# Optimization experiments

Hardware: AMD Instinct MI355X
Metric: run time of the kernel (lower is better)

The kernel has to match this reference:

```python
import jax, jax.numpy as jnp
import numpy as np

N = 50000
E = 1600000
F_IN = 512
H1, C1 = 8, 8          # layer1: 8 heads x 8 channels, concat -> 64
C2 = 40                # layer2: 1 head, num_classes
NEG_SLOPE = 0.2


def setup_inputs() -> dict:
    key = jax.random.key(0)
    ks = jax.random.split(key, 12)
    x = jax.random.normal(ks[0], (N, F_IN), dtype=jnp.float32)
    edge_index = jax.random.randint(ks[1], (2, E), 0, N, dtype=jnp.int32)
    s1 = 1.0 / np.sqrt(F_IN)
    W1 = jax.random.uniform(ks[2], (F_IN, H1 * C1), jnp.float32, -s1, s1)
    att_src1 = jax.random.normal(ks[3], (1, H1, C1), dtype=jnp.float32) * 0.1
    att_dst1 = jax.random.normal(ks[4], (1, H1, C1), dtype=jnp.float32) * 0.1
    b1 = jnp.zeros((H1 * C1,), jnp.float32)
    s2 = 1.0 / np.sqrt(H1 * C1)
    W2 = jax.random.uniform(ks[5], (H1 * C1, C2), jnp.float32, -s2, s2)
    att_src2 = jax.random.normal(ks[6], (1, 1, C2), dtype=jnp.float32) * 0.1
    att_dst2 = jax.random.normal(ks[7], (1, 1, C2), dtype=jnp.float32) * 0.1
    b2 = jnp.zeros((C2,), jnp.float32)
    return {"x": x, "edge_index": edge_index,
            "W1": W1, "att_src1": att_src1, "att_dst1": att_dst1, "b1": b1,
            "W2": W2, "att_src2": att_src2, "att_dst2": att_dst2, "b2": b2}


def gat_conv(x, W, att_src, att_dst, bias, src, dst, heads, out_ch, concat):
    n = x.shape[0]
    h = (x @ W).reshape(n, heads, out_ch)                 # [N,H,C]
    a_src = (h * att_src).sum(-1)                          # [N,H]
    a_dst = (h * att_dst).sum(-1)                          # [N,H]
    logits = jax.nn.leaky_relu(a_src[src] + a_dst[dst], NEG_SLOPE)  # [E,H]
    # segment softmax over incoming edges per destination node
    m = jax.ops.segment_max(logits, dst, num_segments=n)   # [N,H]
    ex = jnp.exp(logits - m[dst])                          # [E,H]
    denom = jax.ops.segment_sum(ex, dst, num_segments=n)   # [N,H]
    w = ex / denom[dst]                                    # [E,H]
    out = jax.ops.segment_sum(h[src] * w[:, :, None], dst, num_segments=n)  # [N,H,C]
    if concat:
        out = out.reshape(n, heads * out_ch)
    else:
        out = out.mean(axis=1)
    return out + bias


def reference(x, edge_index, W1, att_src1, att_dst1, b1, W2, att_src2, att_dst2, b2):
    # add self loops (PyG add_self_loops=True)
    loop = jnp.arange(N, dtype=edge_index.dtype)
    src = jnp.concatenate([edge_index[0], loop])
    dst = jnp.concatenate([edge_index[1], loop])
    # dropout is identity in eval mode
    h = gat_conv(x, W1, att_src1, att_dst1, b1, src, dst, H1, C1, True)
    h = jax.nn.relu(h)
    h = gat_conv(h, W2, att_src2, att_dst2, b2, src, dst, 1, C2, False)
    return jax.nn.log_softmax(h, axis=1)
```

## Files before the change

### kernel.cpp

```cpp
#include <hip/hip_runtime.h>
#include <math.h>

#define NN 50000
#define EE 1600000
#define FIN 512
#define H1N 8
#define C2N 40
#define NEG 0.2f

#define NB 391
#define CAPG 6144
#define PA_ITEMS 8192
#define NITEMS (EE + NN)
#define PA_BLOCKS ((NITEMS + PA_ITEMS - 1) / PA_ITEMS)

__global__ __launch_bounds__(256) void passA_kernel(const int* __restrict__ ei,
    int* __restrict__ bucket_cnt, unsigned int* __restrict__ bucket_glob) {
  __shared__ int hist[NB];
  __shared__ int prefix[NB];
  __shared__ int cursor[NB];
  __shared__ int gbase[NB];
  __shared__ int scA[512], scB[512];
  __shared__ unsigned int staging[PA_ITEMS];
  int t = threadIdx.x;
  int i0 = blockIdx.x * PA_ITEMS;
  int count = NITEMS - i0; if (count > PA_ITEMS) count = PA_ITEMS;

  for (int b = t; b < NB; b += 256) hist[b] = 0;
  __syncthreads();
  for (int j = t; j < count; j += 256) {
    int e = i0 + j;
    int dst = (e < EE) ? ei[EE + e] : (e - EE);
    atomicAdd(&hist[dst >> 7], 1);
  }
  __syncthreads();
  scA[t]       = (t < NB) ? hist[t] : 0;
  scA[t + 256] = (t + 256 < NB) ? hist[t + 256] : 0;
  __syncthreads();
  {
    int* pa = scA; int* pb = scB;
    for (int off = 1; off < 512; off <<= 1) {
      pb[t]       = pa[t]       + (t >= off ? pa[t - off] : 0);
      pb[t + 256] = pa[t + 256] + (t + 256 >= off ? pa[t + 256 - off] : 0);
      __syncthreads();
      int* tmp = pa; pa = pb; pb = tmp;
    }
    for (int b = t; b < NB; b += 256) {
      int ex = pa[b] - hist[b];
      prefix[b] = ex;
      cursor[b] = ex;
      if (hist[b] > 0) gbase[b] = atomicAdd(&bucket_cnt[b], hist[b]);
    }
  }
  __syncthreads();
  for (int j = t; j < count; j += 256) {
    int e = i0 + j;
    int src, dst;
    if (e < EE) { src = ei[e]; dst = ei[EE + e]; }
    else        { src = e - EE; dst = src; }
    int b = dst >> 7;
    unsigned int v = (unsigned int)src | ((unsigned int)(dst & 127) << 16)
                   | ((unsigned int)b << 23);
    int lp = atomicAdd(&cursor[b], 1);
    staging[lp] = v;
  }
  __syncthreads();
  for (int j = t; j < count; j += 256) {
    unsigned int v = staging[j];
    int b = (int)(v >> 23);
    int gpos = b * CAPG + gbase[b] + (j - prefix[b]);
    bucket_glob[gpos] = v;
  }
}

__global__ __launch_bounds__(512) void scan_buckets(const int* __restrict__ bucket_cnt,
    int* __restrict__ bucket_base, int* __restrict__ row_ptr_last) {
  __shared__ int scA[512], scB[512];
  int t = threadIdx.x;
  int v = (t < NB) ? bucket_cnt[t] : 0;
  scA[t] = v;
  __syncthreads();
  int* pa = scA; int* pb = scB;
  for (int off = 1; off < 512; off <<= 1) {
    pb[t] = pa[t] + (t >= off ? pa[t - off] : 0);
    __syncthreads();
    int* tmp = pa; pa = pb; pb = tmp;
  }
  if (t < NB) bucket_base[t] = pa[t] - v;
  if (t == NB - 1) *row_ptr_last = pa[t];
}

#define CAPB 6144
__global__ __launch_bounds__(256) void passB_kernel(const unsigned int* __restrict__ bucket_glob,
    const int* __restrict__ bucket_cnt, const int* __restrict__ bucket_base,
    int* __restrict__ row_ptr, int* __restrict__ col) {
  __shared__ int hist[128], pre[128], cur[128];
  __shared__ int scA[128], scB[128];
  __shared__ int sorted[CAPB];
  int b = blockIdx.x, t = threadIdx.x;
  int cnt = bucket_cnt[b];
  int base = bucket_base[b];
  const unsigned int* in = bucket_glob + (size_t)b * CAPG;
  if (t < 128) hist[t] = 0;
  __syncthreads();
  for (int j = t; j < cnt; j += 256) {
    int dl = (int)((in[j] >> 16) & 127u);
    atomicAdd(&hist[dl], 1);
  }
  __syncthreads();
  if (t < 128) scA[t] = hist[t];
  __syncthreads();
  {
    int* pa = scA; int* pb = scB;
    for (int off = 1; off < 128; off <<= 1) {
      if (t < 128) pb[t] = pa[t] + (t >= off ? pa[t - off] : 0);
      __syncthreads();
      int* tmp = pa; pa = pb; pb = tmp;
    }
    if (t < 128) {
      int ex = pa[t] - hist[t];
      pre[t] = ex;
      cur[t] = ex;
      int d = b * 128 + t;
      if (d < NN) row_ptr[d] = base + ex;
    }
  }
  __syncthreads();
  for (int j = t; j < cnt; j += 256) {
    unsigned int v = in[j];
    int dl = (int)((v >> 16) & 127u);
    int lp = atomicAdd(&cur[dl], 1);
    sorted[lp] = (int)(v & 0xFFFFu);
  }
  __syncthreads();
  for (int j = t; j < cnt; j += 256) col[base + j] = sorted[j];
}


typedef __attribute__((ext_vector_type(8))) short bf16x8;
typedef __attribute__((ext_vector_type(4))) float f32x4;

__device__ inline short f2bf(float f) {
  unsigned int u = __float_as_uint(f);
  u += 0x7FFFu + ((u >> 16) & 1u);
  return (short)(u >> 16);
}
__device__ inline unsigned int pack2bf(float lo, float hi) {
  return (unsigned int)(unsigned short)f2bf(lo) | ((unsigned int)(unsigned short)f2bf(hi) << 16);
}
__device__ inline float bflo(unsigned int v) { return __uint_as_float(v << 16); }
__device__ inline float bfhi(unsigned int v) { return __uint_as_float(v & 0xFFFF0000u); }


__global__ void w1t_kernel(const float* __restrict__ W, short* __restrict__ WT) {
  int i = blockIdx.x * 256 + threadIdx.x;
  if (i >= 64 * 512) return;
  int n = i >> 9, k = i & 511;
  WT[i] = f2bf(W[k * 64 + n]);
}

#define XS_STRIDE 136
__global__ __launch_bounds__(256) void gemm1_kernel(const float* __restrict__ x,
    const short* __restrict__ WT, unsigned short* __restrict__ h1b) {
  __shared__ short xs[64 * XS_STRIDE];
  int t = threadIdx.x;
  int wave = t >> 6, lane = t & 63;
  int quad = lane >> 4, m = lane & 15;
  int row0 = blockIdx.x * 64;
  f32x4 acc[4] = {{0.f,0.f,0.f,0.f},{0.f,0.f,0.f,0.f},{0.f,0.f,0.f,0.f},{0.f,0.f,0.f,0.f}};
  for (int kc = 0; kc < 4; ++kc) {
    int k0 = kc * 128;
    __syncthreads();
#pragma unroll
    for (int jj = 0; jj < 8; ++jj) {
      int idx = jj * 256 + t;
      int row = idx >> 5, kq = idx & 31;
      int rr = row0 + row; if (rr >= NN) rr = NN - 1;
      float4 v = *(const float4*)(x + (size_t)rr * FIN + k0 + kq * 4);
      short4 s;
      s.x = f2bf(v.x); s.y = f2bf(v.y); s.z = f2bf(v.z); s.w = f2bf(v.w);
      *(short4*)&xs[row * XS_STRIDE + kq * 4] = s;
    }
    __syncthreads();
#pragma unroll
    for (int ks = 0; ks < 4; ++ks) {
      bf16x8 a = *(bf16x8*)&xs[(wave * 16 + m) * XS_STRIDE + ks * 32 + quad * 8];
#pragma unroll
      for (int tl = 0; tl < 4; ++tl) {
        bf16x8 b = *(const bf16x8*)(WT + (size_t)(tl * 16 + m) * 512 + k0 + ks * 32 + quad * 8);
        acc[tl] = __builtin_amdgcn_mfma_f32_16x16x32_bf16(a, b, acc[tl], 0, 0, 0);
      }
    }
  }
  int rbase = row0 + wave * 16 + quad * 4;
#pragma unroll
  for (int tl = 0; tl < 4; ++tl) {
#pragma unroll
    for (int r = 0; r < 4; ++r) {
      int rr = rbase + r;
      if (rr < NN) h1b[(size_t)rr * 64 + tl * 16 + m] = (unsigned short)f2bf(acc[tl][r]);
    }
  }
}


__global__ void att1_kernel(const unsigned int* __restrict__ h1b, const float* __restrict__ att_src,
    const float* __restrict__ att_dst, float* __restrict__ asrc, float* __restrict__ adst) {
  int i = blockIdx.x * blockDim.x + threadIdx.x;
  if (i >= NN * H1N) return;
  int h = i & 7;
  uint4 v = *(const uint4*)(h1b + (size_t)i * 4);
  float f[8] = {bflo(v.x), bfhi(v.x), bflo(v.y), bfhi(v.y),
                bflo(v.z), bfhi(v.z), bflo(v.w), bfhi(v.w)};
  const float* as = att_src + h * 8;
  const float* ad = att_dst + h * 8;
  float s = 0.f, d = 0.f;
#pragma unroll
  for (int c = 0; c < 8; ++c) { s = fmaf(f[c], as[c], s); d = fmaf(f[c], ad[c], d); }
  asrc[i] = s;
  adst[i] = d;
}


__global__ __launch_bounds__(256) void l1_edge_kernel(const int* __restrict__ row_ptr,
    const int* __restrict__ col, const unsigned int* __restrict__ h1b,
    const float* __restrict__ asrc, const float* __restrict__ adst,
    const float* __restrict__ b1, float* __restrict__ hrelu) {
  int d = (blockIdx.x * blockDim.x + threadIdx.x) >> 6;
  int lane = threadIdx.x & 63;
  if (d >= NN) return;
  int half = lane >> 5, c2 = lane & 31, h = c2 >> 2;
  int start = row_ptr[d], end = row_ptr[d + 1];
  float adst_h = adst[d * 8 + h];
  float ax = 0.f, ay = 0.f, den = 0.f;
  int e = start;
  int n8 = start + ((end - start) & ~7);
  for (; e < n8; e += 8) {
    int s[4];
#pragma unroll
    for (int j = 0; j < 4; ++j) s[j] = col[e + 2 * j + half];
    float av[4];
#pragma unroll
    for (int j = 0; j < 4; ++j) av[j] = asrc[s[j] * 8 + h];
    unsigned int hv[4];
#pragma unroll
    for (int j = 0; j < 4; ++j) hv[j] = h1b[(size_t)s[j] * 32 + c2];
#pragma unroll
    for (int j = 0; j < 4; ++j) {
      float a = av[j] + adst_h;
      float logit = a > 0.f ? a : NEG * a;
      float ex = __expf(logit);
      den += ex;
      ax = fmaf(ex, bflo(hv[j]), ax);
      ay = fmaf(ex, bfhi(hv[j]), ay);
    }
  }
  for (; e + 1 < end; e += 2) {
    int s = col[e + half];
    float a = asrc[s * 8 + h] + adst_h;
    float logit = a > 0.f ? a : NEG * a;
    float ex = __expf(logit);
    unsigned int hv = h1b[(size_t)s * 32 + c2];
    den += ex;
    ax = fmaf(ex, bflo(hv), ax);
    ay = fmaf(ex, bfhi(hv), ay);
  }
  if (e < end) {
    int s = col[e];
    float a = asrc[s * 8 + h] + adst_h;
    float logit = a > 0.f ? a : NEG * a;
    float ex = (half == 0) ? __expf(logit) : 0.f;
    unsigned int hv = h1b[(size_t)s * 32 + c2];
    den += ex;
    ax = fmaf(ex, bflo(hv), ax);
    ay = fmaf(ex, bfhi(hv), ay);
  }
  ax += __shfl_xor(ax, 32);
  ay += __shfl_xor(ay, 32);
  den += __shfl_xor(den, 32);
  if (half == 0) {
    float inv = 1.f / den;
    float o0 = fmaxf(fmaf(ax, inv, 0.f) + b1[2 * c2], 0.f);
    float o1 = fmaxf(fmaf(ay, inv, 0.f) + b1[2 * c2 + 1], 0.f);
    *(float2*)(hrelu + (size_t)d * 64 + 2 * c2) = make_float2(o0, o1);
  }
}


__global__ __launch_bounds__(256) void gemm2_kernel(const float* __restrict__ hrelu,
    const float* __restrict__ W2, unsigned int* __restrict__ gb) {
  __shared__ float w2s[64 * C2N];
  for (int i = threadIdx.x; i < 64 * C2N; i += 256) w2s[i] = W2[i];
  __syncthreads();
  int idx = blockIdx.x * 256 + threadIdx.x;
  if (idx >= NN * 20) return;
  int n = idx / 20;
  int c2 = idx - n * 20;
  const float* hr = hrelu + (size_t)n * 64;
  float a0 = 0.f, a1 = 0.f;
#pragma unroll
  for (int k = 0; k < 64; ++k) {
    float hv = hr[k];
    a0 = fmaf(hv, w2s[k * C2N + 2 * c2], a0);
    a1 = fmaf(hv, w2s[k * C2N + 2 * c2 + 1], a1);
  }
  gb[idx] = pack2bf(a0, a1);
}


__global__ __launch_bounds__(256) void att2_kernel(const unsigned int* __restrict__ gb,
    const float* __restrict__ att_src, const float* __restrict__ att_dst,
    float* __restrict__ asrc2, float* __restrict__ adst2) {
  int wv = (blockIdx.x * blockDim.x + threadIdx.x) >> 6;
  int lane = threadIdx.x & 63;
  if (wv >= NN) return;
  float as = 0.f, ad = 0.f;
  if (lane < 20) {
    unsigned int v = gb[(size_t)wv * 20 + lane];
    float f0 = bflo(v), f1 = bfhi(v);
    as = f0 * att_src[2 * lane] + f1 * att_src[2 * lane + 1];
    ad = f0 * att_dst[2 * lane] + f1 * att_dst[2 * lane + 1];
  }
#pragma unroll
  for (int off = 16; off >= 1; off >>= 1) {
    as += __shfl_xor(as, off);
    ad += __shfl_xor(ad, off);
  }
  if (lane == 0) { asrc2[wv] = as; adst2[wv] = ad; }
}


__global__ __launch_bounds__(256) void l2_edge_kernel(const int* __restrict__ row_ptr,
    const int* __restrict__ col, const unsigned int* __restrict__ gb,
    const float* __restrict__ asrc2, const float* __restrict__ adst2,
    const float* __restrict__ b2, float* __restrict__ out) {
  int d = (blockIdx.x * blockDim.x + threadIdx.x) >> 6;
  int lane = threadIdx.x & 63;
  if (d >= NN) return;
  int half = lane >> 5, c2 = lane & 31;
  bool act = c2 < 20;
  int start = row_ptr[d], end = row_ptr[d + 1];
  float adst_d = adst2[d];
  float ax = 0.f, ay = 0.f, den = 0.f;
  int e = start;
  int n8 = start + ((end - start) & ~7);
  for (; e < n8; e += 8) {
    int s[4];
#pragma unroll
    for (int j = 0; j < 4; ++j) s[j] = col[e + 2 * j + half];
    float av[4];
#pragma unroll
    for (int j = 0; j < 4; ++j) av[j] = asrc2[s[j]];
    unsigned int gv[4];
#pragma unroll
    for (int j = 0; j < 4; ++j) gv[j] = gb[(size_t)s[j] * 20 + c2];
#pragma unroll
    for (int j = 0; j < 4; ++j) {
      float a = av[j] + adst_d;
      float logit = a > 0.f ? a : NEG * a;
      float ex = __expf(logit);
      den += ex;
      ax = fmaf(ex, bflo(gv[j]), ax);
      ay = fmaf(ex, bfhi(gv[j]), ay);
    }
  }
  for (; e + 1 < end; e += 2) {
    int s = col[e + half];
    float a = asrc2[s] + adst_d;
    float logit = a > 0.f ? a : NEG * a;
    float ex = __expf(logit);
    unsigned int gv = gb[(size_t)s * 20 + c2];
    den += ex;
    ax = fmaf(ex, bflo(gv), ax);
    ay = fmaf(ex, bfhi(gv), ay);
  }
  if (e < end) {
    int s = col[e];
    float a = asrc2[s] + adst_d;
    float logit = a > 0.f ? a : NEG * a;
    float ex = (half == 0) ? __expf(logit) : 0.f;
    unsigned int gv = gb[(size_t)s * 20 + c2];
    den += ex;
    ax = fmaf(ex, bflo(gv), ax);
    ay = fmaf(ex, bfhi(gv), ay);
  }
  ax += __shfl_xor(ax, 32);
  ay += __shfl_xor(ay, 32);
  den += __shfl_xor(den, 32);
  float inv = 1.f / den;
  float o0 = act ? fmaf(ax, inv, 0.f) + b2[2 * c2]     : 0.f;
  float o1 = act ? fmaf(ay, inv, 0.f) + b2[2 * c2 + 1] : 0.f;
  float m = act ? fmaxf(o0, o1) : -INFINITY;
#pragma unroll
  for (int off = 16; off >= 1; off >>= 1) m = fmaxf(m, __shfl_xor(m, off));
  float es = act ? (__expf(o0 - m) + __expf(o1 - m)) : 0.f;
#pragma unroll
  for (int off = 16; off >= 1; off >>= 1) es += __shfl_xor(es, off);
  float ls = logf(es);
  if (act && half == 0)
    *(float2*)(out + (size_t)d * C2N + 2 * c2) = make_float2(o0 - m - ls, o1 - m - ls);
}


extern "C" void kernel_launch(void* const* d_in, const int* in_sizes, int n_in,
                              void* d_out, int out_size, void* d_ws, size_t ws_size,
                              hipStream_t stream) {
  const float* x        = (const float*)d_in[0];
  const int*   ei       = (const int*)d_in[1];
  const float* W1       = (const float*)d_in[2];
  const float* att_src1 = (const float*)d_in[3];
  const float* att_dst1 = (const float*)d_in[4];
  const float* b1       = (const float*)d_in[5];
  const float* W2       = (const float*)d_in[6];
  const float* att_src2 = (const float*)d_in[7];
  const float* att_dst2 = (const float*)d_in[8];
  const float* b2       = (const float*)d_in[9];
  float* out = (float*)d_out;

  char* ws = (char*)d_ws;
  size_t off = 0;
  auto alloc = [&](size_t n_elem) {
    void* p = ws + off;
    off = (off + n_elem * 4 + 255) & ~(size_t)255;
    return p;
  };
  unsigned int* h1b = (unsigned int*)alloc((size_t)NN * 32);
  float* hrelu = (float*)alloc((size_t)NN * 64);
  unsigned int* gb  = (unsigned int*)alloc((size_t)NN * 20 + 16);
  float* asrc1 = (float*)alloc((size_t)NN * 8);
  float* adst1 = (float*)alloc((size_t)NN * 8);
  float* asrc2 = (float*)alloc(NN);
  float* adst2 = (float*)alloc(NN);
  int* row_ptr = (int*)alloc(NN + 1);
  int* colv    = (int*)alloc(EE + NN);
  int* bucket_cnt  = (int*)alloc(NB);
  int* bucket_base = (int*)alloc(NB);
  short* w1t   = (short*)alloc(64 * 512 / 2);
  unsigned int* bucket_glob = (unsigned int*)hrelu;

  hipMemsetAsync(bucket_cnt, 0, NB * 4, stream);
  passA_kernel<<<PA_BLOCKS, 256, 0, stream>>>(ei, bucket_cnt, bucket_glob);
  scan_buckets<<<1, 512, 0, stream>>>(bucket_cnt, bucket_base, row_ptr + NN);
  passB_kernel<<<NB, 256, 0, stream>>>(bucket_glob, bucket_cnt, bucket_base, row_ptr, colv);

  w1t_kernel<<<(64 * 512 + 255) / 256, 256, 0, stream>>>(W1, w1t);
  gemm1_kernel<<<(NN + 63) / 64, 256, 0, stream>>>(x, w1t, (unsigned short*)h1b);
  att1_kernel<<<(NN * 8 + 255) / 256, 256, 0, stream>>>(h1b, att_src1, att_dst1, asrc1, adst1);
  l1_edge_kernel<<<(NN * 64 + 255) / 256, 256, 0, stream>>>(row_ptr, colv, h1b, asrc1, adst1, b1, hrelu);

  gemm2_kernel<<<(NN * 20 + 255) / 256, 256, 0, stream>>>(hrelu, W2, gb);
  att2_kernel<<<(NN * 64 + 255) / 256, 256, 0, stream>>>(gb, att_src2, att_dst2, asrc2, adst2);
  l2_edge_kernel<<<(NN * 64 + 255) / 256, 256, 0, stream>>>(row_ptr, colv, gb, asrc2, adst2, b2, out);
}
```

Before: 367.8 us.

## Fuse attention projections and layer-2 GEMM into neighboring kernels

Folds the W1 transpose into extra blocks of the edge-bucketing kernel. The layer-1 attention dot products move into the gemm1 epilogue through a shared-memory staging tile. The layer-2 dense projection and its attention scores are computed per destination node inside the layer-1 edge kernel, so the hrelu intermediate and three launches go away. This removes global round trips and launch overhead. In exchange, the edge kernel carries extra shared memory and a W2 load per block, and the bucket buffer now needs its own workspace allocation.

```diff
diff --git a/kernel.cpp b/kernel.cpp
--- a/kernel.cpp
+++ b/kernel.cpp
@@ -13,16 +13,42 @@
 #define PA_ITEMS 8192
 #define NITEMS (EE + NN)
 #define PA_BLOCKS ((NITEMS + PA_ITEMS - 1) / PA_ITEMS)
+#define W1T_BLOCKS 32
+
+typedef __attribute__((ext_vector_type(8))) short bf16x8;
+typedef __attribute__((ext_vector_type(4))) float f32x4;
+
+__device__ inline short f2bf(float f) {
+  unsigned int u = __float_as_uint(f);
+  u += 0x7FFFu + ((u >> 16) & 1u);
+  return (short)(u >> 16);
+}
+__device__ inline unsigned int pack2bf(float lo, float hi) {
+  return (unsigned int)(unsigned short)f2bf(lo) | ((unsigned int)(unsigned short)f2bf(hi) << 16);
+}
+__device__ inline float bflo(unsigned int v) { return __uint_as_float(v << 16); }
+__device__ inline float bfhi(unsigned int v) { return __uint_as_float(v & 0xFFFF0000u); }
 
 __global__ __launch_bounds__(256) void passA_kernel(const int* __restrict__ ei,
-    int* __restrict__ bucket_cnt, unsigned int* __restrict__ bucket_glob) {
+    int* __restrict__ bucket_cnt, unsigned int* __restrict__ bucket_glob,
+    const float* __restrict__ W1, short* __restrict__ WT) {
+  int t = threadIdx.x;
+  if (blockIdx.x >= PA_BLOCKS) {
+    int base = (blockIdx.x - PA_BLOCKS) * 1024 + t * 4;
+#pragma unroll
+    for (int j = 0; j < 4; ++j) {
+      int i = base + j;
+      int n = i >> 9, k = i & 511;
+      WT[i] = f2bf(W1[k * 64 + n]);
+    }
+    return;
+  }
   __shared__ int hist[NB];
   __shared__ int prefix[NB];
   __shared__ int cursor[NB];
   __shared__ int gbase[NB];
   __shared__ int scA[512], scB[512];
   __shared__ unsigned int staging[PA_ITEMS];
-  int t = threadIdx.x;
   int i0 = blockIdx.x * PA_ITEMS;
   int count = NITEMS - i0; if (count > PA_ITEMS) count = PA_ITEMS;
 
@@ -137,32 +163,15 @@
 }
 
 
-typedef __attribute__((ext_vector_type(8))) short bf16x8;
-typedef __attribute__((ext_vector_type(4))) float f32x4;
-
-__device__ inline short f2bf(float f) {
-  unsigned int u = __float_as_uint(f);
-  u += 0x7FFFu + ((u >> 16) & 1u);
-  return (short)(u >> 16);
-}
-__device__ inline unsigned int pack2bf(float lo, float hi) {
-  return (unsigned int)(unsigned short)f2bf(lo) | ((unsigned int)(unsigned short)f2bf(hi) << 16);
-}
-__device__ inline float bflo(unsigned int v) { return __uint_as_float(v << 16); }
-__device__ inline float bfhi(unsigned int v) { return __uint_as_float(v & 0xFFFF0000u); }
-
-
-__global__ void w1t_kernel(const float* __restrict__ W, short* __restrict__ WT) {
-  int i = blockIdx.x * 256 + threadIdx.x;
-  if (i >= 64 * 512) return;
-  int n = i >> 9, k = i & 511;
-  WT[i] = f2bf(W[k * 64 + n]);
-}
-
 #define XS_STRIDE 136
+#define HS_STRIDE 68
 __global__ __launch_bounds__(256) void gemm1_kernel(const float* __restrict__ x,
-    const short* __restrict__ WT, unsigned short* __restrict__ h1b) {
-  __shared__ short xs[64 * XS_STRIDE];
+    const short* __restrict__ WT, unsigned short* __restrict__ h1b,
+    const float* __restrict__ att_src, const float* __restrict__ att_dst,
+    float* __restrict__ asrc, float* __restrict__ adst) {
+  __shared__ char smem[64 * XS_STRIDE * 2];
+  short* xs = (short*)smem;
+  float* hsf = (float*)smem;
   int t = threadIdx.x;
   int wave = t >> 6, lane = t & 63;
   int quad = lane >> 4, m = lane & 15;
@@ -192,43 +201,52 @@
       }
     }
   }
-  int rbase = row0 + wave * 16 + quad * 4;
+  __syncthreads();
+  int rl0 = wave * 16 + quad * 4;
 #pragma unroll
   for (int tl = 0; tl < 4; ++tl) {
 #pragma unroll
     for (int r = 0; r < 4; ++r) {
-      int rr = rbase + r;
+      int rr = row0 + rl0 + r;
       if (rr < NN) h1b[(size_t)rr * 64 + tl * 16 + m] = (unsigned short)f2bf(acc[tl][r]);
-    }
-  }
-}
-
-
-__global__ void att1_kernel(const unsigned int* __restrict__ h1b, const float* __restrict__ att_src,
-    const float* __restrict__ att_dst, float* __restrict__ asrc, float* __restrict__ adst) {
-  int i = blockIdx.x * blockDim.x + threadIdx.x;
-  if (i >= NN * H1N) return;
-  int h = i & 7;
-  uint4 v = *(const uint4*)(h1b + (size_t)i * 4);
-  float f[8] = {bflo(v.x), bfhi(v.x), bflo(v.y), bfhi(v.y),
-                bflo(v.z), bfhi(v.z), bflo(v.w), bfhi(v.w)};
-  const float* as = att_src + h * 8;
-  const float* ad = att_dst + h * 8;
-  float s = 0.f, d = 0.f;
-#pragma unroll
-  for (int c = 0; c < 8; ++c) { s = fmaf(f[c], as[c], s); d = fmaf(f[c], ad[c], d); }
-  asrc[i] = s;
-  adst[i] = d;
+      hsf[(rl0 + r) * HS_STRIDE + tl * 16 + m] = acc[tl][r];
+    }
+  }
+  __syncthreads();
+#pragma unroll
+  for (int p = 0; p < 2; ++p) {
+    int idx = p * 256 + t;
+    int rl = idx >> 3, h = idx & 7;
+    int rr = row0 + rl;
+    if (rr < NN) {
+      const float* hv = &hsf[rl * HS_STRIDE + h * 8];
+      const float* as = att_src + h * 8;
+      const float* ad = att_dst + h * 8;
+      float s = 0.f, dd = 0.f;
+#pragma unroll
+      for (int c = 0; c < 8; ++c) { s = fmaf(hv[c], as[c], s); dd = fmaf(hv[c], ad[c], dd); }
+      asrc[rr * 8 + h] = s;
+      adst[rr * 8 + h] = dd;
+    }
+  }
 }
 
 
 __global__ __launch_bounds__(256) void l1_edge_kernel(const int* __restrict__ row_ptr,
     const int* __restrict__ col, const unsigned int* __restrict__ h1b,
     const float* __restrict__ asrc, const float* __restrict__ adst,
-    const float* __restrict__ b1, float* __restrict__ hrelu) {
-  int d = (blockIdx.x * blockDim.x + threadIdx.x) >> 6;
-  int lane = threadIdx.x & 63;
-  if (d >= NN) return;
+    const float* __restrict__ b1, const float* __restrict__ W2,
+    const float* __restrict__ att_src2, const float* __restrict__ att_dst2,
+    unsigned int* __restrict__ gb, float* __restrict__ asrc2, float* __restrict__ adst2) {
+  __shared__ float w2s[64 * C2N];
+  __shared__ float hs[4][64];
+  __shared__ float gs[4][48];
+  int t = threadIdx.x;
+  for (int i = t; i < 64 * C2N; i += 256) w2s[i] = W2[i];
+  __syncthreads();
+  int d = (blockIdx.x * 256 + t) >> 6;
+  int lane = t & 63;
+  int wave = t >> 6;
   int half = lane >> 5, c2 = lane & 31, h = c2 >> 2;
   int start = row_ptr[d], end = row_ptr[d + 1];
   float adst_h = adst[d * 8 + h];
@@ -282,51 +300,25 @@
     float inv = 1.f / den;
     float o0 = fmaxf(fmaf(ax, inv, 0.f) + b1[2 * c2], 0.f);
     float o1 = fmaxf(fmaf(ay, inv, 0.f) + b1[2 * c2 + 1], 0.f);
-    *(float2*)(hrelu + (size_t)d * 64 + 2 * c2) = make_float2(o0, o1);
-  }
-}
-
-
-__global__ __launch_bounds__(256) void gemm2_kernel(const float* __restrict__ hrelu,
-    const float* __restrict__ W2, unsigned int* __restrict__ gb) {
-  __shared__ float w2s[64 * C2N];
-  for (int i = threadIdx.x; i < 64 * C2N; i += 256) w2s[i] = W2[i];
-  __syncthreads();
-  int idx = blockIdx.x * 256 + threadIdx.x;
-  if (idx >= NN * 20) return;
-  int n = idx / 20;
-  int c2 = idx - n * 20;
-  const float* hr = hrelu + (size_t)n * 64;
-  float a0 = 0.f, a1 = 0.f;
-#pragma unroll
-  for (int k = 0; k < 64; ++k) {
-    float hv = hr[k];
-    a0 = fmaf(hv, w2s[k * C2N + 2 * c2], a0);
-    a1 = fmaf(hv, w2s[k * C2N + 2 * c2 + 1], a1);
-  }
-  gb[idx] = pack2bf(a0, a1);
-}
-
-
-__global__ __launch_bounds__(256) void att2_kernel(const unsigned int* __restrict__ gb,
-    const float* __restrict__ att_src, const float* __restrict__ att_dst,
-    float* __restrict__ asrc2, float* __restrict__ adst2) {
-  int wv = (blockIdx.x * blockDim.x + threadIdx.x) >> 6;
-  int lane = threadIdx.x & 63;
-  if (wv >= NN) return;
-  float as = 0.f, ad = 0.f;
-  if (lane < 20) {
-    unsigned int v = gb[(size_t)wv * 20 + lane];
-    float f0 = bflo(v), f1 = bfhi(v);
-    as = f0 * att_src[2 * lane] + f1 * att_src[2 * lane + 1];
-    ad = f0 * att_dst[2 * lane] + f1 * att_dst[2 * lane + 1];
-  }
-#pragma unroll
-  for (int off = 16; off >= 1; off >>= 1) {
-    as += __shfl_xor(as, off);
-    ad += __shfl_xor(ad, off);
-  }
-  if (lane == 0) { asrc2[wv] = as; adst2[wv] = ad; }
+    hs[wave][2 * c2]     = o0;
+    hs[wave][2 * c2 + 1] = o1;
+  }
+  int c = lane;
+  float gacc = 0.f;
+  if (c < C2N) {
+#pragma unroll
+    for (int k = 0; k < 64; ++k) gacc = fmaf(hs[wave][k], w2s[k * C2N + c], gacc);
+  }
+  float asv = (c < C2N) ? gacc * att_src2[c] : 0.f;
+  float adv = (c < C2N) ? gacc * att_dst2[c] : 0.f;
+#pragma unroll
+  for (int off = 32; off >= 1; off >>= 1) {
+    asv += __shfl_xor(asv, off);
+    adv += __shfl_xor(adv, off);
+  }
+  if (lane == 0) { asrc2[d] = asv; adst2[d] = adv; }
+  if (c < C2N) gs[wave][c] = gacc;
+  if (lane < 20) gb[(size_t)d * 20 + lane] = pack2bf(gs[wave][2 * lane], gs[wave][2 * lane + 1]);
 }
 
 
@@ -339,6 +331,7 @@
   if (d >= NN) return;
   int half = lane >> 5, c2 = lane & 31;
   bool act = c2 < 20;
+  int cL = act ? c2 : 19;
   int start = row_ptr[d], end = row_ptr[d + 1];
   float adst_d = adst2[d];
   float ax = 0.f, ay = 0.f, den = 0.f;
@@ -353,7 +346,7 @@
     for (int j = 0; j < 4; ++j) av[j] = asrc2[s[j]];
     unsigned int gv[4];
 #pragma unroll
-    for (int j = 0; j < 4; ++j) gv[j] = gb[(size_t)s[j] * 20 + c2];
+    for (int j = 0; j < 4; ++j) gv[j] = gb[(size_t)s[j] * 20 + cL];
 #pragma unroll
     for (int j = 0; j < 4; ++j) {
       float a = av[j] + adst_d;
@@ -369,7 +362,7 @@
     float a = asrc2[s] + adst_d;
     float logit = a > 0.f ? a : NEG * a;
     float ex = __expf(logit);
-    unsigned int gv = gb[(size_t)s * 20 + c2];
+    unsigned int gv = gb[(size_t)s * 20 + cL];
     den += ex;
     ax = fmaf(ex, bflo(gv), ax);
     ay = fmaf(ex, bfhi(gv), ay);
@@ -379,7 +372,7 @@
     float a = asrc2[s] + adst_d;
     float logit = a > 0.f ? a : NEG * a;
     float ex = (half == 0) ? __expf(logit) : 0.f;
-    unsigned int gv = gb[(size_t)s * 20 + c2];
+    unsigned int gv = gb[(size_t)s * 20 + cL];
     den += ex;
     ax = fmaf(ex, bflo(gv), ax);
     ay = fmaf(ex, bfhi(gv), ay);
@@ -425,8 +418,8 @@
     return p;
   };
   unsigned int* h1b = (unsigned int*)alloc((size_t)NN * 32);
-  float* hrelu = (float*)alloc((size_t)NN * 64);
   unsigned int* gb  = (unsigned int*)alloc((size_t)NN * 20 + 16);
+  unsigned int* bucket_glob = (unsigned int*)alloc((size_t)NB * CAPG);
   float* asrc1 = (float*)alloc((size_t)NN * 8);
   float* adst1 = (float*)alloc((size_t)NN * 8);
   float* asrc2 = (float*)alloc(NN);
@@ -436,19 +429,16 @@
   int* bucket_cnt  = (int*)alloc(NB);
   int* bucket_base = (int*)alloc(NB);
   short* w1t   = (short*)alloc(64 * 512 / 2);
-  unsigned int* bucket_glob = (unsigned int*)hrelu;
 
   hipMemsetAsync(bucket_cnt, 0, NB * 4, stream);
-  passA_kernel<<<PA_BLOCKS, 256, 0, stream>>>(ei, bucket_cnt, bucket_glob);
+  passA_kernel<<<PA_BLOCKS + W1T_BLOCKS, 256, 0, stream>>>(ei, bucket_cnt, bucket_glob, W1, w1t);
   scan_buckets<<<1, 512, 0, stream>>>(bucket_cnt, bucket_base, row_ptr + NN);
   passB_kernel<<<NB, 256, 0, stream>>>(bucket_glob, bucket_cnt, bucket_base, row_ptr, colv);
 
-  w1t_kernel<<<(64 * 512 + 255) / 256, 256, 0, stream>>>(W1, w1t);
-  gemm1_kernel<<<(NN + 63) / 64, 256, 0, stream>>>(x, w1t, (unsigned short*)h1b);
-  att1_kernel<<<(NN * 8 + 255) / 256, 256, 0, stream>>>(h1b, att_src1, att_dst1, asrc1, adst1);
-  l1_edge_kernel<<<(NN * 64 + 255) / 256, 256, 0, stream>>>(row_ptr, colv, h1b, asrc1, adst1, b1, hrelu);
-
-  gemm2_kernel<<<(NN * 20 + 255) / 256, 256, 0, stream>>>(hrelu, W2, gb);
-  att2_kernel<<<(NN * 64 + 255) / 256, 256, 0, stream>>>(gb, att_src2, att_dst2, asrc2, adst2);
+  gemm1_kernel<<<(NN + 63) / 64, 256, 0, stream>>>(x, w1t, (unsigned short*)h1b,
+                                                   att_src1, att_dst1, asrc1, adst1);
+  l1_edge_kernel<<<(NN * 64 + 255) / 256, 256, 0, stream>>>(row_ptr, colv, h1b, asrc1, adst1,
+                                                            b1, W2, att_src2, att_dst2,
+                                                            gb, asrc2, adst2);
   l2_edge_kernel<<<(NN * 64 + 255) / 256, 256, 0, stream>>>(row_ptr, colv, gb, asrc2, adst2, b2, out);
 }
```

Measured after the change: 360.1 us. 2.1% less time.
